# Optimization experiments

Measured on AMD Instinct MI355X. Metric: run time of the kernel, lower is better.

## Reference

```python
import jax, jax.numpy as jnp
import numpy as np

B, S, E = 4, 1024, 1024
H, DK, HS = 16, 64, 64
FF = 4096
EPS = 1e-6


def _layernorm(x, g, b):
    mu = jnp.mean(x, axis=-1, keepdims=True)
    var = jnp.mean((x - mu) ** 2, axis=-1, keepdims=True)
    return (x - mu) * jax.lax.rsqrt(var + EPS) * g + b


def setup_inputs() -> dict:
    key = jax.random.key(0)
    ks = jax.random.split(key, 20)
    s_e = 1.0 / np.sqrt(E)
    s_ff = 1.0 / np.sqrt(FF)
    d = {
        "x": jax.random.normal(ks[0], (B, S, E), jnp.float32),
        "pos_encoding": jax.random.normal(ks[1], (S, S, 8), jnp.float32),
        # weights stored [in, out] (torch Linear transposed)
        "Wq": jax.random.normal(ks[2], (E, H * DK), jnp.float32) * s_e,
        "bq": jnp.zeros((H * DK,), jnp.float32),
        "Wk": jax.random.normal(ks[3], (E, H * DK), jnp.float32) * s_e,
        "bk": jnp.zeros((H * DK,), jnp.float32),
        "Wv": jax.random.normal(ks[4], (E, H * HS), jnp.float32) * s_e,
        "bv": jnp.zeros((H * HS,), jnp.float32),
        "Wo": jax.random.normal(ks[5], (H * HS, E), jnp.float32) * s_e,
        "bo": jnp.zeros((E,), jnp.float32),
        "Wg": jax.random.normal(ks[6], (E, E), jnp.float32) * s_e,
        "bg": jnp.zeros((E,), jnp.float32),
        "Wf1": jax.random.normal(ks[7], (E, FF), jnp.float32) * s_e,
        "bf1": jnp.zeros((FF,), jnp.float32),
        "Wfg": jax.random.normal(ks[8], (E, FF), jnp.float32) * s_e,
        "bfg": jnp.zeros((FF,), jnp.float32),
        "Wf2": jax.random.normal(ks[9], (FF, E), jnp.float32) * s_ff,
        "bf2": jnp.zeros((E,), jnp.float32),
        "ln1_g": jnp.ones((E,), jnp.float32),
        "ln1_b": jnp.zeros((E,), jnp.float32),
        "ln2_g": jnp.ones((E,), jnp.float32),
        "ln2_b": jnp.zeros((E,), jnp.float32),
    }
    return d


def reference(x, pos_encoding, Wq, bq, Wk, bk, Wv, bv, Wo, bo, Wg, bg,
              Wf1, bf1, Wfg, bfg, Wf2, bf2, ln1_g, ln1_b, ln2_g, ln2_b):
    b, s, _ = x.shape
    q = (x @ Wq + bq).reshape(b, s, H, DK)
    k = (x @ Wk + bk).reshape(b, s, H, DK)
    v = (x @ Wv + bv).reshape(b, s, H, HS)
    scale = jnp.sqrt(jnp.float32(DK))
    # [b, h, q, k]
    scores = jnp.einsum("bqhd,bkhd->bhqk", q, k) / scale
    pos_bias = jnp.mean(pos_encoding[:s, :s, :], axis=-1)  # [s, s]
    scores = scores + pos_bias[None, None, :, :]
    probs = jax.nn.softmax(scores, axis=-1)
    ctx = jnp.einsum("bhqk,bkhd->bqhd", probs, v).reshape(b, s, H * HS)
    attn_out = ctx @ Wo + bo
    attn_out = jax.nn.sigmoid(x @ Wg + bg) * attn_out
    x1 = _layernorm(x + attn_out, ln1_g, ln1_b)
    ff = (x1 @ Wf1 + bf1) * jax.nn.sigmoid(x1 @ Wfg + bfg)
    ff = ff @ Wf2 + bf2
    return _layernorm(x1 + ff, ln2_g, ln2_b)
```

## Files before the change

kernel.cpp:

```cpp
#include <hip/hip_runtime.h>

constexpr int NB = 4, NS = 1024, NE = 1024, NH = 16, NFF = 4096;
constexpr int NM = NB * NS;

typedef short s8v __attribute__((ext_vector_type(8)));
typedef short s4v __attribute__((ext_vector_type(4)));
typedef float f4  __attribute__((ext_vector_type(4)));

__device__ __forceinline__ float b2f(unsigned short u) {
    union { unsigned int i; float f; } v; v.i = ((unsigned int)u) << 16; return v.f;
}
__device__ __forceinline__ unsigned short f2b(float f) {
    union { float f; unsigned int i; } v; v.f = f;
    unsigned int r = v.i + 0x7FFFu + ((v.i >> 16) & 1u);
    return (unsigned short)(r >> 16);
}
__device__ __forceinline__ float sigf(float x) { return 1.f / (1.f + __expf(-x)); }

#define GL2LDS(g, l) __builtin_amdgcn_global_load_lds( \
    (const __attribute__((address_space(1))) void*)(g), \
    (__attribute__((address_space(3))) void*)(l), 16, 0, 0)

__global__ __launch_bounds__(256) void cvt_x_kernel(
    const float* __restrict__ X, unsigned short* __restrict__ O)
{
    size_t i = ((size_t)blockIdx.x * 256 + threadIdx.x) * 8;
    f4 v0 = *(const f4*)(X + i), v1 = *(const f4*)(X + i + 4);
    s8v o;
#pragma unroll
    for (int j = 0; j < 4; j++) { o[j] = (short)f2b(v0[j]); o[4 + j] = (short)f2b(v1[j]); }
    *(s8v*)(O + i) = o;
}

__global__ __launch_bounds__(256) void cvt_t_kernel(
    const float* s0, const float* s1, const float* s2, const float* s3, const float* s4,
    unsigned short* d0, unsigned short* d1, unsigned short* d2, unsigned short* d3,
    unsigned short* d4, int K, int N)
{
    const int z = blockIdx.z;
    const float* W = (z == 0) ? s0 : (z == 1) ? s1 : (z == 2) ? s2 : (z == 3) ? s3 : s4;
    unsigned short* WT = (z == 0) ? d0 : (z == 1) ? d1 : (z == 2) ? d2 : (z == 3) ? d3 : d4;
    __shared__ unsigned short L[64][72];
    const int k0 = blockIdx.y * 64, n0 = blockIdx.x * 64;
    const int t = threadIdx.x;
    const int r = t >> 4, c4 = (t & 15) * 4;
#pragma unroll
    for (int p = 0; p < 4; p++) {
        int k = r + p * 16;
        f4 v = *(const f4*)&W[(size_t)(k0 + k) * N + n0 + c4];
#pragma unroll
        for (int i = 0; i < 4; i++) L[c4 + i][k] = f2b(v[i]);
    }
    __syncthreads();
    const int n = t >> 2, kc = (t & 3) * 16;
    s8v o0, o1;
#pragma unroll
    for (int i = 0; i < 8; i++) { o0[i] = (short)L[n][kc + i]; o1[i] = (short)L[n][kc + 8 + i]; }
    unsigned short* dst = WT + (size_t)(n0 + n) * K + k0 + kc;
    *(s8v*)dst = o0; *(s8v*)(dst + 8) = o1;
}

__global__ __launch_bounds__(256) void posmean_kernel(
    const float* __restrict__ pe, float* __restrict__ bias)
{
    int idx = blockIdx.x * 256 + threadIdx.x;
    const float* p = pe + (size_t)idx * 8;
    f4 v0 = *(const f4*)p, v1 = *(const f4*)(p + 4);
    float s = 0.f;
#pragma unroll
    for (int i = 0; i < 4; i++) s += v0[i] + v1[i];
    bias[idx] = (s * 0.125f - 8.0f) * 1.44269504f;
}

#define EPI_QKVG     0
#define EPI_GATE_RES 2
#define EPI_RES      4
#define EPI_BIAS     5

template <int EPI, int TM>
__global__ __launch_bounds__(256) void gemm_bt(
    const unsigned short* __restrict__ A,
    const unsigned short* __restrict__ BT,
    const float* b0p, const float* b1p, const float* b2p, const float* b3p,
    const unsigned short* ex1,
    const unsigned short* ex2,
    unsigned short* C, int M, int N, int K)
{
    constexpr int AR = 32 * TM;
    __shared__ short As0[AR * 32], As1[AR * 32];
    __shared__ short Bs0[128 * 32], Bs1[128 * 32];

    const int tid  = threadIdx.x;
    const int m0   = blockIdx.y * AR;
    const int n0   = blockIdx.x * 128;
    const int lane = tid & 63;
    const int wave = tid >> 6;
    const int wm   = (wave >> 1) * (16 * TM), wn = (wave & 1) * 64;
    const int quad = lane >> 4, lo = lane & 15;
    const int lrow = lane >> 2;
    const int lcol = (((lane & 3) ^ ((lane >> 4) & 3))) * 8;
    const int rcol = ((quad ^ ((lo >> 2) & 3))) * 8;

    f4 acc[TM][4];
#pragma unroll
    for (int i = 0; i < TM; i++)
#pragma unroll
        for (int j = 0; j < 4; j++)
#pragma unroll
            for (int r = 0; r < 4; r++) acc[i][j][r] = 0.f;

    const unsigned short* ga = A  + (size_t)(m0 + wave * (AR / 4) + lrow) * K + lcol;
    const unsigned short* gb = BT + (size_t)(n0 + wave * 32 + lrow) * K + lcol;
    short* lA0  = &As0[(wave * (AR / 4)) * 32];
    short* lA1  = &As1[(wave * (AR / 4)) * 32];
    short* lB00 = &Bs0[(wave * 32) * 32];
    short* lB01 = &Bs0[(wave * 32 + 16) * 32];
    short* lB10 = &Bs1[(wave * 32) * 32];
    short* lB11 = &Bs1[(wave * 32 + 16) * 32];

    for (int k0 = 0; k0 < K; k0 += 64) {
#pragma unroll
        for (int t = 0; t < TM / 2; t++) {
            GL2LDS(ga + k0 +      (size_t)t * 16 * K, lA0 + t * 16 * 32);
            GL2LDS(ga + k0 + 32 + (size_t)t * 16 * K, lA1 + t * 16 * 32);
        }
        GL2LDS(gb + k0,               lB00);
        GL2LDS(gb + k0 + 16 * K,      lB01);
        GL2LDS(gb + k0 + 32,          lB10);
        GL2LDS(gb + k0 + 32 + 16 * K, lB11);
        __syncthreads();

        s8v af[TM], bf[4];
#pragma unroll
        for (int i = 0; i < TM; i++)
            af[i] = *(const s8v*)&As0[(wm + i * 16 + lo) * 32 + rcol];
#pragma unroll
        for (int j = 0; j < 4; j++)
            bf[j] = *(const s8v*)&Bs0[(wn + j * 16 + lo) * 32 + rcol];
#pragma unroll
        for (int i = 0; i < TM; i++)
#pragma unroll
            for (int j = 0; j < 4; j++)
                acc[i][j] = __builtin_amdgcn_mfma_f32_16x16x32_bf16(af[i], bf[j], acc[i][j], 0, 0, 0);
#pragma unroll
        for (int i = 0; i < TM; i++)
            af[i] = *(const s8v*)&As1[(wm + i * 16 + lo) * 32 + rcol];
#pragma unroll
        for (int j = 0; j < 4; j++)
            bf[j] = *(const s8v*)&Bs1[(wn + j * 16 + lo) * 32 + rcol];
#pragma unroll
        for (int i = 0; i < TM; i++)
#pragma unroll
            for (int j = 0; j < 4; j++)
                acc[i][j] = __builtin_amdgcn_mfma_f32_16x16x32_bf16(af[i], bf[j], acc[i][j], 0, 0, 0);
        __syncthreads();
    }

    const float* bp = b0p;
    bool do_sig = false;
    if (EPI == EPI_QKVG) {
        int seg = n0 >> 10;
        bp = (seg == 0) ? b0p : (seg == 1) ? b1p : (seg == 2) ? b2p : b3p;
        do_sig = (n0 >= 3072);
    }

#pragma unroll
    for (int i = 0; i < TM; i++) {
#pragma unroll
        for (int j = 0; j < 4; j++) {
#pragma unroll
            for (int r = 0; r < 4; r++) {
                int gm = m0 + wm + i * 16 + quad * 4 + r;
                int gn = n0 + wn + j * 16 + lo;
                size_t idx = (size_t)gm * N + gn;
                float v = acc[i][j][r] + (EPI == EPI_QKVG ? bp[gn & 1023] : bp[gn]);
                if (EPI == EPI_QKVG)          { if (do_sig) v = sigf(v); }
                else if (EPI == EPI_GATE_RES) v = b2f(ex1[idx]) + b2f(ex2[(size_t)gm * 4096 + gn]) * v;
                else if (EPI == EPI_RES)      v = b2f(ex1[idx]) + v;
                C[idx] = f2b(v);
            }
        }
    }
}

__global__ __launch_bounds__(512, 1) void gemm_ff8(
    const unsigned short* __restrict__ A,
    const unsigned short* __restrict__ B1T,
    const unsigned short* __restrict__ B2T,
    const float* __restrict__ bias1, const float* __restrict__ bias2,
    unsigned short* __restrict__ C)
{
    __shared__ short Lds[8 * 8192];

    const int tid  = threadIdx.x;
    const int ln   = tid & 63, wv = tid >> 6;
    const int wr   = wv >> 1, wc = wv & 1;
    const int quad = ln >> 4, lo = ln & 15;
    const int m0   = blockIdx.y * 256, n0 = blockIdx.x * 128;

    const int rowst = wv * 8 + (ln >> 3);
    const int cosrc = ((ln & 7) ^ (ln >> 3)) * 8;
    short* const ldst0 = &Lds[(wv * 8) * 64];

    f4 accA[4][4], accB[4][4];
#pragma unroll
    for (int i = 0; i < 4; i++)
#pragma unroll
        for (int j = 0; j < 4; j++)
#pragma unroll
            for (int r = 0; r < 4; r++) { accA[i][j][r] = 0.f; accB[i][j][r] = 0.f; }

    auto stage_half = [&](int h) {
        if (h >= 64) return;
        const int tt = h >> 2, kind = h & 3, slot = h & 7;
        const unsigned short* gsrc;
        if (kind == 0)      gsrc = A   + (size_t)(m0 + rowst) * 1024 + tt * 64 + cosrc;
        else if (kind == 1) gsrc = A   + (size_t)(m0 + 128 + rowst) * 1024 + tt * 64 + cosrc;
        else if (kind == 2) gsrc = B1T + (size_t)(n0 + rowst) * 1024 + tt * 64 + cosrc;
        else                gsrc = B2T + (size_t)(n0 + rowst) * 1024 + tt * 64 + cosrc;
        short* ldst = ldst0 + slot * 8192;
        GL2LDS(gsrc,                     ldst);
        GL2LDS(gsrc + (size_t)64 * 1024, ldst + 64 * 64);
    };

    int aoff[2], boff[2];
#pragma unroll
    for (int kh = 0; kh < 2; kh++) {
        const int sw = (((kh * 4 + quad) ^ (lo & 7)) * 8);
        aoff[kh] = (((wr & 1) * 64 + lo) * 64) + sw;
        boff[kh] = ((wc * 64 + lo) * 64) + sw;
    }
    const int slA = wr >> 1;

#pragma unroll
    for (int h = 0; h < 5; h++) stage_half(h);
    asm volatile("s_waitcnt vmcnt(2)" ::: "memory");
    __builtin_amdgcn_s_barrier();

    for (int t = 0; t < 16; t++) {
        const int p4 = (t & 1) * 4;
        const short* LA  = &Lds[(p4 + slA) * 8192];
        const short* LB1 = &Lds[(p4 + 2) * 8192];
        const short* LB2 = &Lds[(p4 + 3) * 8192];
        const int hb = 4 * t;
        s8v af[4], bf[4];

#pragma unroll
        for (int i = 0; i < 4; i++) af[i] = *(const s8v*)&LA[aoff[0] + i * 1024];
#pragma unroll
        for (int j = 0; j < 4; j++) bf[j] = *(const s8v*)&LB1[boff[0] + j * 1024];
        stage_half(hb + 5);
        __builtin_amdgcn_s_barrier();
        __builtin_amdgcn_s_setprio(1);
#pragma unroll
        for (int i = 0; i < 4; i++)
#pragma unroll
            for (int j = 0; j < 4; j++)
                accA[i][j] = __builtin_amdgcn_mfma_f32_16x16x32_bf16(af[i], bf[j], accA[i][j], 0, 0, 0);
        __builtin_amdgcn_s_setprio(0);
        __builtin_amdgcn_s_barrier();

#pragma unroll
        for (int j = 0; j < 4; j++) bf[j] = *(const s8v*)&LB2[boff[0] + j * 1024];
        stage_half(hb + 6);
        __builtin_amdgcn_s_barrier();
        __builtin_amdgcn_s_setprio(1);
#pragma unroll
        for (int i = 0; i < 4; i++)
#pragma unroll
            for (int j = 0; j < 4; j++)
                accB[i][j] = __builtin_amdgcn_mfma_f32_16x16x32_bf16(af[i], bf[j], accB[i][j], 0, 0, 0);
        __builtin_amdgcn_s_setprio(0);
        __builtin_amdgcn_s_barrier();

#pragma unroll
        for (int i = 0; i < 4; i++) af[i] = *(const s8v*)&LA[aoff[1] + i * 1024];
#pragma unroll
        for (int j = 0; j < 4; j++) bf[j] = *(const s8v*)&LB1[boff[1] + j * 1024];
        stage_half(hb + 7);
        __builtin_amdgcn_s_barrier();
        __builtin_amdgcn_s_setprio(1);
#pragma unroll
        for (int i = 0; i < 4; i++)
#pragma unroll
            for (int j = 0; j < 4; j++)
                accA[i][j] = __builtin_amdgcn_mfma_f32_16x16x32_bf16(af[i], bf[j], accA[i][j], 0, 0, 0);
        __builtin_amdgcn_s_setprio(0);
        __builtin_amdgcn_s_barrier();

#pragma unroll
        for (int j = 0; j < 4; j++) bf[j] = *(const s8v*)&LB2[boff[1] + j * 1024];
        stage_half(hb + 8);
        __builtin_amdgcn_s_barrier();
        __builtin_amdgcn_s_setprio(1);
#pragma unroll
        for (int i = 0; i < 4; i++)
#pragma unroll
            for (int j = 0; j < 4; j++)
                accB[i][j] = __builtin_amdgcn_mfma_f32_16x16x32_bf16(af[i], bf[j], accB[i][j], 0, 0, 0);
        __builtin_amdgcn_s_setprio(0);
        if (t < 14)       { asm volatile("s_waitcnt vmcnt(2)" ::: "memory"); }
        else if (t == 14) { asm volatile("s_waitcnt vmcnt(0)" ::: "memory"); }
        __builtin_amdgcn_s_barrier();
    }

#pragma unroll
    for (int i = 0; i < 4; i++) {
#pragma unroll
        for (int j = 0; j < 4; j++) {
#pragma unroll
            for (int r = 0; r < 4; r++) {
                int gm = m0 + wr * 64 + i * 16 + quad * 4 + r;
                int gn = n0 + wc * 64 + j * 16 + lo;
                float a = accA[i][j][r] + bias1[gn];
                float g = accB[i][j][r] + bias2[gn];
                C[(size_t)gm * 4096 + gn] = f2b(a * sigf(g));
            }
        }
    }
}

__global__ __launch_bounds__(256) void attn_kernel(
    const unsigned short* __restrict__ QKVG, const float* __restrict__ bias,
    unsigned short* __restrict__ ctx)
{
    __shared__ short Ks[32 * 72];
    __shared__ short Vt[64 * 48];
    __shared__ short Ps[4][16 * 40];

    const int tid = threadIdx.x;
    const int lane = tid & 63, wave = tid >> 6;
    const int quad = lane >> 4, lo = lane & 15;
    const int bh = blockIdx.y;
    const int b = bh >> 4, h = bh & 15;
    const int q0 = blockIdx.x * 64 + wave * 16;
    const size_t base  = (size_t)b * NS * 4096 + (size_t)h * 64;
    const size_t baseK = base + 1024, baseV = base + 2048;
    constexpr float c1 = 0.125f * 1.44269504f;

    s8v aq0 = *(const s8v*)(QKVG + base + (size_t)(q0 + lo) * 4096 + quad * 8);
    s8v aq1 = *(const s8v*)(QKVG + base + (size_t)(q0 + lo) * 4096 + 32 + quad * 8);

    f4 accO[4];
    float l_r[4];
#pragma unroll
    for (int r = 0; r < 4; r++) {
        l_r[r] = 0.f;
#pragma unroll
        for (int j = 0; j < 4; j++) accO[j][r] = 0.f;
    }

    const int skv = tid >> 3, sd8 = (tid & 7) * 8;
    const int vkv = tid & 31, vd8 = (tid >> 5) * 8;
    const int pvk = 2 * (vkv & 15) + (vkv >> 4);

    s8v kk = *(const s8v*)(QKVG + baseK + (size_t)skv * 4096 + sd8);
    s8v vv = *(const s8v*)(QKVG + baseV + (size_t)vkv * 4096 + vd8);

    for (int kv0 = 0; kv0 < NS; kv0 += 32) {
        *(s8v*)&Ks[skv * 72 + sd8] = kk;
#pragma unroll
        for (int i = 0; i < 8; i++) Vt[(vd8 + i) * 48 + pvk] = (short)vv[i];
        __syncthreads();

        s8v kkn = kk, vvn = vv;
        if (kv0 + 32 < NS) {
            kkn = *(const s8v*)(QKVG + baseK + (size_t)(kv0 + 32 + skv) * 4096 + sd8);
            vvn = *(const s8v*)(QKVG + baseV + (size_t)(kv0 + 32 + vkv) * 4096 + vd8);
        }

        f4 sc[2];
#pragma unroll
        for (int cb = 0; cb < 2; cb++) {
            s8v bk0 = *(const s8v*)&Ks[(cb * 16 + lo) * 72 + quad * 8];
            s8v bk1 = *(const s8v*)&Ks[(cb * 16 + lo) * 72 + 32 + quad * 8];
            f4 z;
#pragma unroll
            for (int r = 0; r < 4; r++) z[r] = 0.f;
            z = __builtin_amdgcn_mfma_f32_16x16x32_bf16(aq0, bk0, z, 0, 0, 0);
            sc[cb] = __builtin_amdgcn_mfma_f32_16x16x32_bf16(aq1, bk1, z, 0, 0, 0);
        }

        int* PsI = (int*)&Ps[wave][0];
#pragma unroll
        for (int r = 0; r < 4; r++) {
            int qrow = q0 + quad * 4 + r;
            const float* bp = &bias[(size_t)qrow * NS + kv0];
            float p0 = exp2f(sc[0][r] * c1 + bp[lo]);
            float p1 = exp2f(sc[1][r] * c1 + bp[16 + lo]);
            l_r[r] += p0 + p1;
            unsigned int pk = (unsigned int)f2b(p0) | ((unsigned int)f2b(p1) << 16);
            PsI[(quad * 4 + r) * 20 + lo] = (int)pk;
        }
        s8v pf = *(const s8v*)&Ps[wave][lo * 40 + quad * 8];
#pragma unroll
        for (int j = 0; j < 4; j++) {
            s8v bv = *(const s8v*)&Vt[(j * 16 + lo) * 48 + quad * 8];
            accO[j] = __builtin_amdgcn_mfma_f32_16x16x32_bf16(pf, bv, accO[j], 0, 0, 0);
        }
        __syncthreads();
        kk = kkn; vv = vvn;
    }

#pragma unroll
    for (int r = 0; r < 4; r++) {
        float l = l_r[r];
#pragma unroll
        for (int d = 1; d < 16; d <<= 1) l += __shfl_xor(l, d, 64);
        l_r[r] = 1.f / l;
    }
#pragma unroll
    for (int j = 0; j < 4; j++)
#pragma unroll
        for (int r = 0; r < 4; r++) {
            int qrow = q0 + quad * 4 + r;
            ctx[((size_t)b * NS + qrow) * 1024 + h * 64 + j * 16 + lo] = f2b(accO[j][r] * l_r[r]);
        }
}

__global__ __launch_bounds__(256) void ln_kernel(
    const unsigned short* __restrict__ X, const float* __restrict__ g,
    const float* __restrict__ bb, void* __restrict__ out, int outF32)
{
    const int row = blockIdx.x;
    const unsigned short* xr = X + (size_t)row * NE;
    s4v xv = *(const s4v*)(xr + threadIdx.x * 4);
    float v[4], s = 0.f, ss = 0.f;
#pragma unroll
    for (int i = 0; i < 4; i++) {
        v[i] = b2f((unsigned short)xv[i]);
        s += v[i]; ss += v[i] * v[i];
    }
#pragma unroll
    for (int d = 1; d < 64; d <<= 1) { s += __shfl_xor(s, d, 64); ss += __shfl_xor(ss, d, 64); }
    __shared__ float red[8];
    int wave = threadIdx.x >> 6, lane = threadIdx.x & 63;
    if (lane == 0) { red[wave] = s; red[4 + wave] = ss; }
    __syncthreads();
    s  = red[0] + red[1] + red[2] + red[3];
    ss = red[4] + red[5] + red[6] + red[7];
    float mu = s * (1.f / NE);
    float var = ss * (1.f / NE) - mu * mu;
    float rstd = rsqrtf(fmaxf(var, 0.f) + 1e-6f);
#pragma unroll
    for (int i = 0; i < 4; i++) {
        int c = threadIdx.x * 4 + i;
        size_t idx = (size_t)row * NE + c;
        float o = (v[i] - mu) * rstd * g[c] + bb[c];
        if (outF32) ((float*)out)[idx] = o;
        else        ((unsigned short*)out)[idx] = f2b(o);
    }
}

extern "C" void kernel_launch(void* const* d_in, const int* in_sizes, int n_in,
                              void* d_out, int out_size, void* d_ws, size_t ws_size,
                              hipStream_t stream)
{
    const float* x    = (const float*)d_in[0];
    const float* pe   = (const float*)d_in[1];
    const float* Wq   = (const float*)d_in[2];
    const float* bq   = (const float*)d_in[3];
    const float* Wk   = (const float*)d_in[4];
    const float* bk   = (const float*)d_in[5];
    const float* Wv   = (const float*)d_in[6];
    const float* bv   = (const float*)d_in[7];
    const float* Wo   = (const float*)d_in[8];
    const float* bo   = (const float*)d_in[9];
    const float* Wg   = (const float*)d_in[10];
    const float* bg   = (const float*)d_in[11];
    const float* Wf1  = (const float*)d_in[12];
    const float* bf1  = (const float*)d_in[13];
    const float* Wfg  = (const float*)d_in[14];
    const float* bfg  = (const float*)d_in[15];
    const float* Wf2  = (const float*)d_in[16];
    const float* bf2  = (const float*)d_in[17];
    const float* ln1g = (const float*)d_in[18];
    const float* ln1b = (const float*)d_in[19];
    const float* ln2g = (const float*)d_in[20];
    const float* ln2b = (const float*)d_in[21];

    char* ws = (char*)d_ws;
    unsigned short* xb    = (unsigned short*)ws;
    unsigned short* WTq   = (unsigned short*)(ws + ( 8ull << 20));
    unsigned short* WoT   = (unsigned short*)(ws + (16ull << 20));
    unsigned short* Wf1T  = (unsigned short*)(ws + (18ull << 20));
    unsigned short* WfgT  = (unsigned short*)(ws + (26ull << 20));
    unsigned short* Wf2T  = (unsigned short*)(ws + (34ull << 20));
    float*          biasP = (float*)(ws + (42ull << 20));
    unsigned short* QKVG  = (unsigned short*)(ws + (46ull << 20));
    unsigned short* T1 = xb;
    unsigned short* Cx = WTq;
    unsigned short* X1 = WTq;
    unsigned short* H1 = QKVG;
    unsigned short* T2 = xb;

    dim3 blk(256);
    cvt_x_kernel<<<dim3(NM * NE / (256 * 8)), blk, 0, stream>>>(x, xb);
    cvt_t_kernel<<<dim3(16, 16, 5), blk, 0, stream>>>(
        Wq, Wk, Wv, Wg, Wo,
        WTq + 0ull * 1024 * 1024, WTq + 1ull * 1024 * 1024,
        WTq + 2ull * 1024 * 1024, WTq + 3ull * 1024 * 1024, WoT, NE, NE);
    cvt_t_kernel<<<dim3(64, 16, 2), blk, 0, stream>>>(
        Wf1, Wfg, nullptr, nullptr, nullptr,
        Wf1T, WfgT, nullptr, nullptr, nullptr, NE, NFF);
    cvt_t_kernel<<<dim3(16, 64, 1), blk, 0, stream>>>(
        Wf2, nullptr, nullptr, nullptr, nullptr,
        Wf2T, nullptr, nullptr, nullptr, nullptr, NFF, NE);
    posmean_kernel<<<dim3(NS * NS / 256), blk, 0, stream>>>(pe, biasP);

    gemm_bt<EPI_QKVG, 4><<<dim3(32, 32), blk, 0, stream>>>(
        xb, WTq, bq, bk, bv, bg, nullptr, nullptr, QKVG, NM, 4096, NE);

    attn_kernel<<<dim3(NS / 64, NB * NH), blk, 0, stream>>>(QKVG, biasP, Cx);

    gemm_bt<EPI_GATE_RES, 2><<<dim3(8, 64), blk, 0, stream>>>(
        Cx, WoT, bo, nullptr, nullptr, nullptr, xb, QKVG + 3072, T1, NM, NE, NE);
    ln_kernel<<<dim3(NM), blk, 0, stream>>>(T1, ln1g, ln1b, X1, 0);

    gemm_ff8<<<dim3(NFF / 128, NM / 256), dim3(512), 0, stream>>>(
        X1, Wf1T, WfgT, bf1, bfg, H1);

    gemm_bt<EPI_RES, 2><<<dim3(8, 64), blk, 0, stream>>>(
        H1, Wf2T, bf2, nullptr, nullptr, nullptr, X1, nullptr, T2, NM, NE, NFF);
    ln_kernel<<<dim3(NM), blk, 0, stream>>>(T2, ln2g, ln2b, d_out, 1);
}
```

Before: 474.1 us.

## Replace QKVG projection GEMM with 256x256-tile 8-wave pipelined kernel

Adds a dedicated QKVG projection kernel that uses 512 threads and 256x256 output tiles. It stages A and B halves directly into LDS through a multi-slot swizzled ring buffer, and interleaves the MFMA phases with barriers and priority hints. The larger tile raises arithmetic intensity and reuse compared with the generic 128x128 gemm_bt, cutting global and L2 traffic for the 4096x4096x1024 projection. In exchange, the grid shrinks to 256 blocks at one block per CU, which risks underfilling the GPU, and the kernel needs many accumulator registers.

```diff
diff --git a/kernel.cpp b/kernel.cpp
--- a/kernel.cpp
+++ b/kernel.cpp
@@ -315,6 +315,145 @@
                 float a = accA[i][j][r] + bias1[gn];
                 float g = accB[i][j][r] + bias2[gn];
                 C[(size_t)gm * 4096 + gn] = f2b(a * sigf(g));
+            }
+        }
+    }
+}
+
+__global__ __launch_bounds__(512, 1) void gemm_qkvg8(
+    const unsigned short* __restrict__ A,
+    const unsigned short* __restrict__ BT,
+    const float* b0p, const float* b1p, const float* b2p, const float* b3p,
+    unsigned short* __restrict__ C)
+{
+    __shared__ short Lds[8 * 8192];
+
+    const int tid  = threadIdx.x;
+    const int ln   = tid & 63, wv = tid >> 6;
+    const int wr   = wv >> 2, wc = wv & 3;
+    const int quad = ln >> 4, lo = ln & 15;
+    const int m0   = blockIdx.y * 256, n0 = blockIdx.x * 256;
+
+    const int rowst = wv * 8 + (ln >> 3);
+    const int cosrc = ((ln & 7) ^ (ln >> 3)) * 8;
+    short* const ldst0 = &Lds[(wv * 8) * 64];
+
+    f4 acc[8][4];
+#pragma unroll
+    for (int i = 0; i < 8; i++)
+#pragma unroll
+        for (int j = 0; j < 4; j++)
+#pragma unroll
+            for (int r = 0; r < 4; r++) acc[i][j][r] = 0.f;
+
+    auto stage_half = [&](int h) {
+        if (h >= 64) return;
+        const int tt = h >> 2, kind = h & 3, slot = h & 7;
+        const unsigned short* gsrc;
+        if (kind == 0)      gsrc = A  + (size_t)(m0 + rowst) * 1024 + tt * 64 + cosrc;
+        else if (kind == 1) gsrc = A  + (size_t)(m0 + 128 + rowst) * 1024 + tt * 64 + cosrc;
+        else if (kind == 2) gsrc = BT + (size_t)(n0 + rowst) * 1024 + tt * 64 + cosrc;
+        else                gsrc = BT + (size_t)(n0 + 128 + rowst) * 1024 + tt * 64 + cosrc;
+        short* ldst = ldst0 + slot * 8192;
+        GL2LDS(gsrc,                     ldst);
+        GL2LDS(gsrc + (size_t)64 * 1024, ldst + 64 * 64);
+    };
+
+    int aoff[2], boff[2];
+#pragma unroll
+    for (int kh = 0; kh < 2; kh++) {
+        const int sw = (((kh * 4 + quad) ^ (lo & 7)) * 8);
+        aoff[kh] = (lo * 64) + sw;
+        boff[kh] = (((wc & 1) * 64 + lo) * 64) + sw;
+    }
+    const int slA = wr;
+    const int slB = 2 + (wc >> 1);
+
+#pragma unroll
+    for (int h = 0; h < 5; h++) stage_half(h);
+    asm volatile("s_waitcnt vmcnt(2)" ::: "memory");
+    __builtin_amdgcn_s_barrier();
+
+    for (int t = 0; t < 16; t++) {
+        const int p4 = (t & 1) * 4;
+        const short* LA = &Lds[(p4 + slA) * 8192];
+        const short* LB = &Lds[(p4 + slB) * 8192];
+        const int hb = 4 * t;
+        s8v af[4], bf[4];
+
+#pragma unroll
+        for (int i = 0; i < 4; i++) af[i] = *(const s8v*)&LA[aoff[0] + i * 1024];
+#pragma unroll
+        for (int j = 0; j < 4; j++) bf[j] = *(const s8v*)&LB[boff[0] + j * 1024];
+        stage_half(hb + 5);
+        __builtin_amdgcn_s_barrier();
+        __builtin_amdgcn_s_setprio(1);
+#pragma unroll
+        for (int i = 0; i < 4; i++)
+#pragma unroll
+            for (int j = 0; j < 4; j++)
+                acc[i][j] = __builtin_amdgcn_mfma_f32_16x16x32_bf16(af[i], bf[j], acc[i][j], 0, 0, 0);
+        __builtin_amdgcn_s_setprio(0);
+        __builtin_amdgcn_s_barrier();
+
+#pragma unroll
+        for (int i = 0; i < 4; i++) af[i] = *(const s8v*)&LA[aoff[0] + (4 + i) * 1024];
+        stage_half(hb + 6);
+        __builtin_amdgcn_s_barrier();
+        __builtin_amdgcn_s_setprio(1);
+#pragma unroll
+        for (int i = 0; i < 4; i++)
+#pragma unroll
+            for (int j = 0; j < 4; j++)
+                acc[4 + i][j] = __builtin_amdgcn_mfma_f32_16x16x32_bf16(af[i], bf[j], acc[4 + i][j], 0, 0, 0);
+        __builtin_amdgcn_s_setprio(0);
+        __builtin_amdgcn_s_barrier();
+
+#pragma unroll
+        for (int i = 0; i < 4; i++) af[i] = *(const s8v*)&LA[aoff[1] + i * 1024];
+#pragma unroll
+        for (int j = 0; j < 4; j++) bf[j] = *(const s8v*)&LB[boff[1] + j * 1024];
+        stage_half(hb + 7);
+        __builtin_amdgcn_s_barrier();
+        __builtin_amdgcn_s_setprio(1);
+#pragma unroll
+        for (int i = 0; i < 4; i++)
+#pragma unroll
+            for (int j = 0; j < 4; j++)
+                acc[i][j] = __builtin_amdgcn_mfma_f32_16x16x32_bf16(af[i], bf[j], acc[i][j], 0, 0, 0);
+        __builtin_amdgcn_s_setprio(0);
+        __builtin_amdgcn_s_barrier();
+
+#pragma unroll
+        for (int i = 0; i < 4; i++) af[i] = *(const s8v*)&LA[aoff[1] + (4 + i) * 1024];
+        stage_half(hb + 8);
+        __builtin_amdgcn_s_barrier();
+        __builtin_amdgcn_s_setprio(1);
+#pragma unroll
+        for (int i = 0; i < 4; i++)
+#pragma unroll
+            for (int j = 0; j < 4; j++)
+                acc[4 + i][j] = __builtin_amdgcn_mfma_f32_16x16x32_bf16(af[i], bf[j], acc[4 + i][j], 0, 0, 0);
+        __builtin_amdgcn_s_setprio(0);
+        if (t < 14)       { asm volatile("s_waitcnt vmcnt(2)" ::: "memory"); }
+        else if (t == 14) { asm volatile("s_waitcnt vmcnt(0)" ::: "memory"); }
+        __builtin_amdgcn_s_barrier();
+    }
+
+    const int seg = n0 >> 10;
+    const float* bp = (seg == 0) ? b0p : (seg == 1) ? b1p : (seg == 2) ? b2p : b3p;
+    const bool do_sig = (n0 >= 3072);
+#pragma unroll
+    for (int i = 0; i < 8; i++) {
+#pragma unroll
+        for (int j = 0; j < 4; j++) {
+#pragma unroll
+            for (int r = 0; r < 4; r++) {
+                int gm = m0 + wr * 128 + i * 16 + quad * 4 + r;
+                int gn = n0 + wc * 64 + j * 16 + lo;
+                float v = acc[i][j][r] + bp[gn & 1023];
+                if (do_sig) v = sigf(v);
+                C[(size_t)gm * 4096 + gn] = f2b(v);
             }
         }
     }
@@ -508,8 +647,8 @@
         Wf2T, nullptr, nullptr, nullptr, nullptr, NFF, NE);
     posmean_kernel<<<dim3(NS * NS / 256), blk, 0, stream>>>(pe, biasP);
 
-    gemm_bt<EPI_QKVG, 4><<<dim3(32, 32), blk, 0, stream>>>(
-        xb, WTq, bq, bk, bv, bg, nullptr, nullptr, QKVG, NM, 4096, NE);
+    gemm_qkvg8<<<dim3(16, 16), dim3(512), 0, stream>>>(
+        xb, WTq, bq, bk, bv, bg, QKVG);
 
     attn_kernel<<<dim3(NS / 64, NB * NH), blk, 0, stream>>>(QKVG, biasP, Cx);
 
```

New measurement: 477.6 us. About the same (+0.7%).
